# Performance work log

Hardware: AMD Instinct MI355X
Metric: run time of the kernel (lower is better)

The kernel has to match this reference:

```python
import jax, jax.numpy as jnp
import numpy as np

B, C, OUT, HD = 2, 256, 256, 32
H = C // HD                      # num_heads = 8
SCALE = HD ** -0.5
N = 40962                        # icosahedron level-6 vertices
N_TOP, TOP = 2562, 16
N_DOWN, DOWN = 2562, 19
M = N_TOP * TOP + N_DOWN * DOWN  # flattened window positions (pad row = index M)
MLP_HID = int(OUT * 2.0)
BN_EPS = 1e-5


def _build_geometry(seed=0):
    rng = np.random.default_rng(seed)
    # every vertex appears at least once; extras create overlapping patches
    flat = np.concatenate([rng.permutation(N), rng.integers(0, N, M - N)]).astype(np.int64)
    top = flat[:N_TOP * TOP].reshape(N_TOP, TOP)
    down = flat[N_TOP * TOP:].reshape(N_DOWN, DOWN)
    counts = np.bincount(flat, minlength=N)
    K = int(counts.max())
    order = np.argsort(flat, kind='stable')
    v_sorted = flat[order]
    cum = np.concatenate([[0], np.cumsum(counts)])
    pos = np.arange(M) - cum[v_sorted]          # within-group rank
    reverse = np.full((N, K), M, dtype=np.int64)  # pad -> zero row
    reverse[v_sorted, pos] = order
    cnt_inv = (1.0 / counts).astype(np.float32)
    return top, down, reverse, cnt_inv


def setup_inputs() -> dict:
    key = jax.random.key(0)
    ks = jax.random.split(key, 8)
    top, down, reverse, cnt_inv = _build_geometry(0)
    s_in, s_out, s_hid = C ** -0.5, OUT ** -0.5, MLP_HID ** -0.5
    return {
        'x': jax.random.normal(ks[0], (B, C, N), jnp.float32),
        'Wqkv': jax.random.normal(ks[1], (C, 3 * C), jnp.float32) * s_in,
        'bqkv': jnp.zeros((3 * C,), jnp.float32),
        'Wproj': jax.random.normal(ks[2], (C, OUT), jnp.float32) * s_in,
        'bproj': jnp.zeros((OUT,), jnp.float32),
        'Wres': jax.random.normal(ks[3], (C, OUT), jnp.float32) * s_in,
        'bres': jnp.zeros((OUT,), jnp.float32),
        'Wm1': jax.random.normal(ks[4], (OUT, MLP_HID), jnp.float32) * s_out,
        'bm1': jnp.zeros((MLP_HID,), jnp.float32),
        'Wm2': jax.random.normal(ks[5], (MLP_HID, OUT), jnp.float32) * s_hid,
        'bm2': jnp.zeros((OUT,), jnp.float32),
        'gamma': jnp.ones((OUT,), jnp.float32),
        'beta': jnp.zeros((OUT,), jnp.float32),
        'cnt_inv': jnp.asarray(cnt_inv),
        'top_idx': jnp.asarray(top),
        'down_idx': jnp.asarray(down),
        'reverse_idx': jnp.asarray(reverse),
    }


def reference(x, Wqkv, bqkv, Wproj, bproj, Wres, bres, Wm1, bm1, Wm2, bm2,
              gamma, beta, cnt_inv, top_idx, down_idx, reverse_idx):
    xt = jnp.transpose(x, (0, 2, 1))                      # B,N,C
    res = xt @ Wres + bres                                # B,N,OUT
    qkv = (xt @ Wqkv + bqkv).reshape(B, N, 3, H, HD)
    qkv = jnp.transpose(qkv, (2, 0, 3, 1, 4))             # 3,B,H,N,hd
    q, k, v = qkv[0] * SCALE, qkv[1], qkv[2]

    def win_attn(idx):
        qw, kw, vw = q[:, :, idx], k[:, :, idx], v[:, :, idx]   # B,H,nw,w,hd
        a = jax.nn.softmax(jnp.einsum('bhnjc,bhnkc->bhnjk', qw, kw), axis=-1)
        return jnp.einsum('bhnjk,bhnkc->bhnjc', a, vw)

    x_top = win_attn(top_idx).reshape(B, H, N_TOP * TOP, HD)
    x_down = win_attn(down_idx).reshape(B, H, N_DOWN * DOWN, HD)
    xw = jnp.concatenate([x_top, x_down], axis=2)         # B,H,M,hd
    xw = jnp.concatenate([xw, jnp.zeros((B, H, 1, HD), xw.dtype)], axis=2)  # pad row
    xg = xw[:, :, reverse_idx, :]                         # B,H,N,K,hd
    xa = (xg * cnt_inv[None, None, :, None, None]).sum(axis=3)  # B,H,N,hd
    xf = jnp.transpose(xa, (0, 2, 1, 3)).reshape(B, N, C)

    out = xf @ Wproj + bproj + res                        # B,N,OUT
    res2 = (out @ Wm1 + bm1) @ Wm2 + bm2                  # no activation (faithful)

    out_t = jnp.transpose(out, (0, 2, 1))                 # B,OUT,N
    r2t = jnp.transpose(res2, (0, 2, 1))
    mean = r2t.mean(axis=(0, 2), keepdims=True)
    var = r2t.var(axis=(0, 2), keepdims=True)             # biased, batch stats
    bn = (r2t - mean) * jax.lax.rsqrt(var + BN_EPS)
    bn = bn * gamma[None, :, None] + beta[None, :, None]
    return out_t + bn
```

## Files before the change

### kernel.cpp

```cpp
#include <hip/hip_runtime.h>
#include <stdint.h>

typedef unsigned short u16;
typedef __bf16 bf16x8 __attribute__((ext_vector_type(8)));
typedef float f32x4 __attribute__((ext_vector_type(4)));

#define B_    2
#define C_    256
#define N_    40962
#define BN_   (B_ * N_)
#define H_    8
#define HD_   32
#define NTOP  2562
#define TOPW  16
#define NDOWN 2562
#define DOWNW 19
#define M_    (NTOP*TOPW + NDOWN*DOWNW)
#define SCALE_ 0.17677669529663687f
#define BN_EPS 1e-5f

__device__ __forceinline__ float b2f(u16 u) {
    union { uint32_t i; float f; } v; v.i = ((uint32_t)u) << 16; return v.f;
}
__device__ __forceinline__ u16 f2b(float f) {
    union { float f; uint32_t i; } v; v.f = f;
    uint32_t r = v.i + 0x7fffu + ((v.i >> 16) & 1u);
    return (u16)(r >> 16);
}
__device__ __forceinline__ float ld(const void* p, size_t i, int isf32) {
    return isf32 ? ((const float*)p)[i] : b2f(((const u16*)p)[i]);
}

__device__ __forceinline__ int xcd_swz_1281(int bx) {
    const int q = 160, r = 1;
    int xcd = bx & 7, o = bx >> 3;
    return (xcd < r ? xcd * (q + 1) : r * (q + 1) + (xcd - r) * q) + o;
}

__global__ void probe_k(const void* __restrict__ x, int* __restrict__ flag) {
    int lane = threadIdx.x;
    u16 v = ((const u16*)x)[2 * lane];
    int e = (v >> 7) & 0xff;
    bool ok = (e >= 118 && e <= 134);
    unsigned long long m = __ballot(ok);
    if (lane == 0) *flag = (__popcll(m) < 32) ? 1 : 0;
}

__global__ void wcat_k(const void* __restrict__ Wqkv, const void* __restrict__ Wres,
                       const void* __restrict__ Wproj,
                       u16* __restrict__ WcatT, u16* __restrict__ WprojT,
                       const int* __restrict__ flag) {
    const int f = *flag;
    int k = blockIdx.x, t = threadIdx.x;
    for (int j = t; j < 768; j += 256) WcatT[(size_t)j * 256 + k] = f2b(ld(Wqkv, (size_t)k * 768 + j, f));
    WcatT[(size_t)(768 + t) * 256 + k] = f2b(ld(Wres, (size_t)k * 256 + t, f));
    WprojT[(size_t)t * 256 + k] = f2b(ld(Wproj, (size_t)k * 256 + t, f));
}

__global__ void biasprep_k(const void* bqkv, const void* bres, const void* bproj,
                           float* bias_cat, float* bias_proj, const int* __restrict__ flag) {
    const int f = *flag;
    int g = blockIdx.x * 256 + threadIdx.x;
    if (g < 768) bias_cat[g] = ld(bqkv, g, f);
    else if (g < 1024) bias_cat[g] = ld(bres, g - 768, f);
    else if (g < 1280) bias_proj[g - 1024] = ld(bproj, g - 1024, f);
}

__global__ __launch_bounds__(256) void wf_k(const void* __restrict__ Wm1, const void* __restrict__ Wm2,
                                            u16* __restrict__ WfT, const int* __restrict__ flag) {
    const int f = *flag;
    __shared__ float row[512];
    int i = blockIdx.x, t = threadIdx.x;
    row[t] = ld(Wm1, (size_t)i * 512 + t, f);
    row[t + 256] = ld(Wm1, (size_t)i * 512 + 256 + t, f);
    __syncthreads();
    float acc = 0.f;
    for (int k = 0; k < 512; ++k) acc += row[k] * ld(Wm2, (size_t)k * 256 + t, f);
    WfT[(size_t)t * 256 + i] = f2b(acc);
}

__global__ void bf_k(const void* bm1, const void* __restrict__ Wm2, const void* bm2,
                     float* bf, const int* __restrict__ flag) {
    const int f = *flag;
    int t = threadIdx.x;
    float acc = ld(bm2, t, f);
    for (int k = 0; k < 512; ++k) acc += ld(bm1, k, f) * ld(Wm2, (size_t)k * 256 + t, f);
    bf[t] = acc;
}

__global__ __launch_bounds__(256) void gemm_qkv_k(
    const void* __restrict__ x, const u16* __restrict__ WcatT,
    const float* __restrict__ bias, u16* __restrict__ Out, const int* __restrict__ flag)
{
    const int isf32 = *flag;
    __shared__ __align__(16) u16 As[64][264];
    const int tid = threadIdx.x;
    const int bx = xcd_swz_1281(blockIdx.x);
    const int R0 = bx * 64;
    const int wave = tid >> 6, lane = tid & 63;
    const int quad = lane >> 4, mrow = lane & 15;

    const bool fastA = (R0 + 64 <= N_) || (R0 >= N_ && R0 + 64 <= BN_);
    if (fastA) {
        const int b = (R0 >= N_) ? 1 : 0;
        const int nn = R0 - b * N_;
        const int k = tid;
        if (isf32) {
            const float* xp = (const float*)x + (size_t)(b * 256 + k) * N_ + nn;
#pragma unroll
            for (int j = 0; j < 32; ++j) {
                float2 v = *reinterpret_cast<const float2*>(xp + 2 * j);
                As[2 * j][k] = f2b(v.x);
                As[2 * j + 1][k] = f2b(v.y);
            }
        } else {
            const u16* xp = (const u16*)x + (size_t)(b * 256 + k) * N_ + nn;
#pragma unroll
            for (int j = 0; j < 32; ++j) {
                uint32_t v = *reinterpret_cast<const uint32_t*>(xp + 2 * j);
                As[2 * j][k] = (u16)v;
                As[2 * j + 1][k] = (u16)(v >> 16);
            }
        }
    } else {
        const int n = tid & 63;
        const int kg = tid >> 6;
        const int g = R0 + n;
        const bool valid = (g < BN_);
        const int b = (g >= N_) ? 1 : 0;
        const int nn = g - b * N_;
#pragma unroll
        for (int j = 0; j < 8; ++j) {
            const int k0 = kg * 8 + j * 32;
            u16 tmp[8];
            if (valid) {
#pragma unroll
                for (int i = 0; i < 8; ++i) tmp[i] = f2b(ld(x, (size_t)(b * 256 + k0 + i) * N_ + nn, isf32));
            } else {
#pragma unroll
                for (int i = 0; i < 8; ++i) tmp[i] = 0;
            }
            *reinterpret_cast<uint4*>(&As[n][k0]) = *reinterpret_cast<const uint4*>(tmp);
        }
    }
    __syncthreads();

    for (int ct = 0; ct < 16; ++ct) {
        const int col = ct * 64 + wave * 16 + mrow;
        const u16* bp = WcatT + (size_t)col * 256 + quad * 8;
        uint4 breg[8];
#pragma unroll
        for (int kc = 0; kc < 8; ++kc) breg[kc] = *reinterpret_cast<const uint4*>(bp + kc * 32);
        f32x4 acc[4] = {f32x4{0,0,0,0}, f32x4{0,0,0,0}, f32x4{0,0,0,0}, f32x4{0,0,0,0}};
#pragma unroll
        for (int kc = 0; kc < 8; ++kc) {
            bf16x8 bfrag = *reinterpret_cast<const bf16x8*>(&breg[kc]);
#pragma unroll
            for (int t2 = 0; t2 < 4; ++t2) {
                bf16x8 afrag = *reinterpret_cast<const bf16x8*>(&As[t2 * 16 + mrow][kc * 32 + quad * 8]);
                acc[t2] = __builtin_amdgcn_mfma_f32_16x16x32_bf16(afrag, bfrag, acc[t2], 0, 0, 0);
            }
        }
        const float bcol = bias[col];
#pragma unroll
        for (int t2 = 0; t2 < 4; ++t2) {
#pragma unroll
            for (int r = 0; r < 4; ++r) {
                int row = R0 + t2 * 16 + quad * 4 + r;
                if (row < BN_) {
                    Out[(size_t)row * 1024 + col] = f2b(acc[t2][r] + bcol);
                }
            }
        }
    }
}

template<bool ADD_RES, bool OUT_F32>
__global__ __launch_bounds__(256) void gemm_k(
    const u16* __restrict__ A, int ldA, const u16* __restrict__ Bt,
    const float* __restrict__ bias,
    const u16* __restrict__ resp, int ldRes,
    void* __restrict__ Out, int ldOut, int Rtot)
{
    __shared__ __align__(16) u16 As[64][264];
    const int tid = threadIdx.x;
    const int bx = xcd_swz_1281(blockIdx.x);
    const int R0 = bx * 64;
    const int wave = tid >> 6, lane = tid & 63;
    const int quad = lane >> 4, mrow = lane & 15;

#pragma unroll
    for (int it = 0; it < 8; ++it) {
        int e = it * 256 + tid;
        int row = e >> 5, ks = (e & 31) * 8;
        uint4 v = make_uint4(0u, 0u, 0u, 0u);
        if (R0 + row < Rtot)
            v = *reinterpret_cast<const uint4*>(A + (size_t)(R0 + row) * ldA + ks);
        *reinterpret_cast<uint4*>(&As[row][ks]) = v;
    }
    __syncthreads();

    for (int ct = 0; ct < 4; ++ct) {
        const int col = ct * 64 + wave * 16 + mrow;
        const u16* bp = Bt + (size_t)col * 256 + quad * 8;
        uint4 breg[8];
#pragma unroll
        for (int kc = 0; kc < 8; ++kc) breg[kc] = *reinterpret_cast<const uint4*>(bp + kc * 32);
        f32x4 acc[4] = {f32x4{0,0,0,0}, f32x4{0,0,0,0}, f32x4{0,0,0,0}, f32x4{0,0,0,0}};
#pragma unroll
        for (int kc = 0; kc < 8; ++kc) {
            bf16x8 bfrag = *reinterpret_cast<const bf16x8*>(&breg[kc]);
#pragma unroll
            for (int t2 = 0; t2 < 4; ++t2) {
                bf16x8 afrag = *reinterpret_cast<const bf16x8*>(&As[t2 * 16 + mrow][kc * 32 + quad * 8]);
                acc[t2] = __builtin_amdgcn_mfma_f32_16x16x32_bf16(afrag, bfrag, acc[t2], 0, 0, 0);
            }
        }
        const float bcol = bias[col];
#pragma unroll
        for (int t2 = 0; t2 < 4; ++t2) {
#pragma unroll
            for (int r = 0; r < 4; ++r) {
                int row = R0 + t2 * 16 + quad * 4 + r;
                if (row < Rtot) {
                    float v = acc[t2][r] + bcol;
                    if (ADD_RES) v += b2f(resp[(size_t)row * ldRes + col]);
                    if (OUT_F32) ((float*)Out)[(size_t)row * ldOut + col] = v;
                    else         ((u16*)Out)[(size_t)row * ldOut + col] = f2b(v);
                }
            }
        }
    }
}

template<int W>
__global__ __launch_bounds__(256) void attn_k(const u16* __restrict__ qkv, const int* __restrict__ widx,
                                              u16* __restrict__ xw, int mbase)
{
    const int w = blockIdx.x, b = blockIdx.y;
    const int tid = threadIdx.x;
    __shared__ int wi[W];
    __shared__ __align__(16) float Ks[W][H_][36];
    __shared__ __align__(16) float Vs[W][H_][36];
    if (tid < W) wi[tid] = widx[w * W + tid];
    __syncthreads();
    for (int e = tid; e < W * 32; e += 256) {
        int j = e >> 5, seg = e & 31;
        size_t base = ((size_t)(b * N_ + wi[j])) * 1024 + 256 + seg * 8;
        uint4 kv = *reinterpret_cast<const uint4*>(qkv + base);
        uint4 vv = *reinterpret_cast<const uint4*>(qkv + base + 256);
        int h = seg >> 2, c0 = (seg & 3) * 8;
        const u16* kp = (const u16*)&kv; const u16* vp = (const u16*)&vv;
#pragma unroll
        for (int t = 0; t < 8; ++t) {
            Ks[j][h][c0 + t] = b2f(kp[t]);
            Vs[j][h][c0 + t] = b2f(vp[t]);
        }
    }
    __syncthreads();

    if (tid < W * H_) {
        const int j = tid >> 3, h = tid & 7;
        float qr[32];
        {
            size_t qb = ((size_t)(b * N_ + wi[j])) * 1024 + h * 32;
#pragma unroll
            for (int s4 = 0; s4 < 4; ++s4) {
                uint4 qv = *reinterpret_cast<const uint4*>(qkv + qb + s4 * 8);
                const u16* qp = (const u16*)&qv;
#pragma unroll
                for (int t = 0; t < 8; ++t) qr[s4 * 8 + t] = b2f(qp[t]) * SCALE_;
            }
        }
        float p[W];
        float mx = -1e30f;
#pragma unroll
        for (int jj = 0; jj < W; ++jj) {
            const float* kr = &Ks[jj][h][0];
            float s = 0.f;
#pragma unroll
            for (int c = 0; c < 32; ++c) s += qr[c] * kr[c];
            p[jj] = s;
            mx = fmaxf(mx, s);
        }
        float sum = 0.f;
#pragma unroll
        for (int jj = 0; jj < W; ++jj) { p[jj] = __expf(p[jj] - mx); sum += p[jj]; }
        const float inv = 1.0f / sum;
        float o[32];
#pragma unroll
        for (int c = 0; c < 32; ++c) o[c] = 0.f;
#pragma unroll
        for (int jj = 0; jj < W; ++jj) {
            const float pj = p[jj];
            const float* vr = &Vs[jj][h][0];
#pragma unroll
            for (int c = 0; c < 32; ++c) o[c] += pj * vr[c];
        }
        const int m = mbase + w * W + j;
        size_t off = ((size_t)b * (M_ + 1) + m) * 256 + h * 32;
#pragma unroll
        for (int s4 = 0; s4 < 4; ++s4) {
            uint32_t w0 = (uint32_t)f2b(o[s4 * 8 + 0] * inv) | ((uint32_t)f2b(o[s4 * 8 + 1] * inv) << 16);
            uint32_t w1 = (uint32_t)f2b(o[s4 * 8 + 2] * inv) | ((uint32_t)f2b(o[s4 * 8 + 3] * inv) << 16);
            uint32_t w2 = (uint32_t)f2b(o[s4 * 8 + 4] * inv) | ((uint32_t)f2b(o[s4 * 8 + 5] * inv) << 16);
            uint32_t w3 = (uint32_t)f2b(o[s4 * 8 + 6] * inv) | ((uint32_t)f2b(o[s4 * 8 + 7] * inv) << 16);
            *reinterpret_cast<uint4*>(xw + off + s4 * 8) = make_uint4(w0, w1, w2, w3);
        }
    }
}

__global__ __launch_bounds__(256) void gather_k(const u16* __restrict__ xw, const int* __restrict__ rev,
                                                const void* __restrict__ cnt_inv, u16* __restrict__ xfp,
                                                int K, const int* __restrict__ flag)
{
    const int f = *flag;
    int gid = blockIdx.x * 4 + (threadIdx.x >> 6);
    if (gid >= BN_) return;
    int b = (gid >= N_) ? 1 : 0;
    int n = gid - b * N_;
    int c4 = (threadIdx.x & 63) * 4;
    float a0 = 0, a1 = 0, a2 = 0, a3 = 0;
    const int* rp = rev + (size_t)n * K;
    for (int k = 0; k < K; ++k) {
        int idx = rp[k];
        if (idx < M_) {
            ushort4 v = *reinterpret_cast<const ushort4*>(xw + ((size_t)b * (M_ + 1) + idx) * 256 + c4);
            a0 += b2f(v.x); a1 += b2f(v.y); a2 += b2f(v.z); a3 += b2f(v.w);
        }
    }
    float ci = ld(cnt_inv, n, f);
    ushort4 o;
    o.x = f2b(a0 * ci); o.y = f2b(a1 * ci); o.z = f2b(a2 * ci); o.w = f2b(a3 * ci);
    *reinterpret_cast<ushort4*>(xfp + (size_t)gid * 1024 + c4) = o;
}

#define STATS_BLOCKS 512
__global__ __launch_bounds__(256) void stats_k(const float* __restrict__ res2, float* __restrict__ sums) {
    const int tid = threadIdx.x;
    const int c4 = (tid & 63) * 4;
    const int rsub = tid >> 6;
    float s[4] = {0.f, 0.f, 0.f, 0.f};
    float q[4] = {0.f, 0.f, 0.f, 0.f};
    for (int r = blockIdx.x * 4 + rsub; r < BN_; r += STATS_BLOCKS * 4) {
        float4 v = *reinterpret_cast<const float4*>(res2 + (size_t)r * 256 + c4);
        s[0] += v.x; q[0] += v.x * v.x;
        s[1] += v.y; q[1] += v.y * v.y;
        s[2] += v.z; q[2] += v.z * v.z;
        s[3] += v.w; q[3] += v.w * v.w;
    }
    __shared__ float rs[256][4];
    __shared__ float rq[256][4];
#pragma unroll
    for (int j = 0; j < 4; ++j) { rs[tid][j] = s[j]; rq[tid][j] = q[j]; }
    __syncthreads();
    if (tid < 64) {
#pragma unroll
        for (int j = 0; j < 4; ++j) {
            float a = rs[tid][j] + rs[tid + 64][j] + rs[tid + 128][j] + rs[tid + 192][j];
            float b = rq[tid][j] + rq[tid + 64][j] + rq[tid + 128][j] + rq[tid + 192][j];
            atomicAdd(&sums[c4 + j], a);
            atomicAdd(&sums[256 + c4 + j], b);
        }
    }
}

__global__ void bnfin_k(const float* sums, const void* gamma, const void* beta, float* ss,
                        const int* __restrict__ flag) {
    const int f = *flag;
    int c = threadIdx.x;
    float mean = sums[c] * (1.0f / BN_);
    float var = sums[256 + c] * (1.0f / BN_) - mean * mean;
    float inv = rsqrtf(fmaxf(var, 0.f) + BN_EPS);
    float sc = ld(gamma, c, f) * inv;
    ss[c] = sc;
    ss[256 + c] = ld(beta, c, f) - mean * sc;
}

__global__ __launch_bounds__(256) void final_k(const u16* __restrict__ outb, const float* __restrict__ res2,
                                               const float* __restrict__ ss, void* __restrict__ y,
                                               const int* __restrict__ flag)
{
    const int isf32 = *flag;
    __shared__ __align__(16) float tile[64][65];
    const int n0 = blockIdx.x * 64, o0 = blockIdx.y * 64, b = blockIdx.z;
    const int tid = threadIdx.x;
    {
        const int ln = tid >> 2, os = (tid & 3) * 16;
        int n = n0 + ln;
        if (n < N_) {
            size_t base = ((size_t)(b * N_ + n)) * 256 + o0 + os;
            uint4 ov0 = *reinterpret_cast<const uint4*>(outb + base);
            uint4 ov1 = *reinterpret_cast<const uint4*>(outb + base + 8);
            const u16* op = (const u16*)&ov0;
            const u16* op1 = (const u16*)&ov1;
            float4 rv[4];
#pragma unroll
            for (int q = 0; q < 4; ++q) rv[q] = *reinterpret_cast<const float4*>(res2 + base + q * 4);
            const float* rp = (const float*)&rv[0];
#pragma unroll
            for (int j = 0; j < 16; ++j) {
                int oc = o0 + os + j;
                float ob = (j < 8) ? b2f(op[j]) : b2f(op1[j - 8]);
                tile[ln][os + j] = ob + rp[j] * ss[oc] + ss[256 + oc];
            }
        }
    }
    __syncthreads();
    {
        const int wave = tid >> 6, lane = tid & 63;
        int n = n0 + lane;
        if (n < N_) {
            if (isf32) {
                float* yp = (float*)y;
#pragma unroll
                for (int r0 = 0; r0 < 64; r0 += 4) {
                    int r = r0 + wave;
                    int oc = o0 + r;
                    yp[((size_t)(b * 256 + oc)) * N_ + n] = tile[lane][r];
                }
            } else {
                u16* yp = (u16*)y;
#pragma unroll
                for (int r0 = 0; r0 < 64; r0 += 4) {
                    int r = r0 + wave;
                    int oc = o0 + r;
                    yp[((size_t)(b * 256 + oc)) * N_ + n] = f2b(tile[lane][r]);
                }
            }
        }
    }
}

static const size_t OFF_QKV   = 0;
static const size_t OFF_XW    = 167780352;
static const size_t OFF_SMALL = 259603456;

extern "C" void kernel_launch(void* const* d_in, const int* in_sizes, int n_in,
                              void* d_out, int out_size, void* d_ws, size_t ws_size,
                              hipStream_t stream) {
    const void* x     = d_in[0];
    const void* Wqkv  = d_in[1];
    const void* bqkv  = d_in[2];
    const void* Wproj = d_in[3];
    const void* bproj = d_in[4];
    const void* Wres  = d_in[5];
    const void* bres  = d_in[6];
    const void* Wm1   = d_in[7];
    const void* bm1   = d_in[8];
    const void* Wm2   = d_in[9];
    const void* bm2   = d_in[10];
    const void* gamma = d_in[11];
    const void* beta  = d_in[12];
    const void* cnt_inv = d_in[13];
    const int* top_idx = (const int*)d_in[14];
    const int* down_idx = (const int*)d_in[15];
    const int* rev   = (const int*)d_in[16];
    const int K = in_sizes[16] / N_;

    char* ws = (char*)d_ws;
    u16*  qkvres  = (u16*)(ws + OFF_QKV);
    float* res2   = (float*)(ws + OFF_QKV);
    u16*  xw      = (u16*)(ws + OFF_XW);
    u16*  outb    = (u16*)(ws + OFF_XW);
    u16*  WcatT   = (u16*)(ws + OFF_SMALL);
    u16*  WfT     = (u16*)(ws + OFF_SMALL + 524288);
    float* bias_cat  = (float*)(ws + OFF_SMALL + 655360);
    float* bias_proj = (float*)(ws + OFF_SMALL + 659456);
    float* bfv       = (float*)(ws + OFF_SMALL + 663552);
    float* stats     = (float*)(ws + OFF_SMALL + 667648);
    float* ssbuf     = (float*)(ws + OFF_SMALL + 671744);
    int*   flag      = (int*)(ws + OFF_SMALL + 675840);
    u16*  WprojT     = (u16*)(ws + OFF_SMALL + 679936);

    probe_k<<<1, 64, 0, stream>>>(x, flag);

    wcat_k<<<256, 256, 0, stream>>>(Wqkv, Wres, Wproj, WcatT, WprojT, flag);
    biasprep_k<<<5, 256, 0, stream>>>(bqkv, bres, bproj, bias_cat, bias_proj, flag);
    wf_k<<<256, 256, 0, stream>>>(Wm1, Wm2, WfT, flag);
    bf_k<<<1, 256, 0, stream>>>(bm1, Wm2, bm2, bfv, flag);

    gemm_qkv_k<<<1281, 256, 0, stream>>>(x, WcatT, bias_cat, qkvres, flag);

    attn_k<TOPW><<<dim3(NTOP, B_), 256, 0, stream>>>(qkvres, top_idx, xw, 0);
    attn_k<DOWNW><<<dim3(NDOWN, B_), 256, 0, stream>>>(qkvres, down_idx, xw, NTOP * TOPW);

    gather_k<<<(BN_ + 3) / 4, 256, 0, stream>>>(xw, rev, cnt_inv, qkvres, K, flag);

    gemm_k<true, false><<<1281, 256, 0, stream>>>(
        qkvres, 1024, WprojT, bias_proj, qkvres + 768, 1024, (void*)outb, 256, BN_);

    gemm_k<false, true><<<1281, 256, 0, stream>>>(
        outb, 256, WfT, bfv, nullptr, 0, (void*)res2, 256, BN_);

    (void)hipMemsetAsync(stats, 0, 512 * sizeof(float), stream);
    stats_k<<<STATS_BLOCKS, 256, 0, stream>>>(res2, stats);
    bnfin_k<<<1, 256, 0, stream>>>(stats, gamma, beta, ssbuf, flag);

    final_k<<<dim3(641, 4, 2), 256, 0, stream>>>(outb, res2, ssbuf, d_out, flag);
}
```

Before: 868.2 us.

## Fuse projection and folded MLP GEMMs into one kernel with paired column tiles

Merges the projection GEMM (plus residual) and the folded MLP GEMM into a single kernel. Each block computes its 64 rows of outb, then reloads them into shared memory and immediately computes res2. This removes one launch and keeps the reload of outb cache-hot. The QKV and fused GEMMs now load B fragments for two column tiles at once to raise memory-level parallelism, at the cost of more registers. res2 is stored with a padded 512-float row stride and offset, which doubles its footprint and may change how its accesses map to channels or banks.

Measured after the change: 981.9 us. 1.13x slower.

```diff
diff --git a/kernel.cpp b/kernel.cpp
--- a/kernel.cpp
+++ b/kernel.cpp
@@ -19,6 +19,8 @@
 #define SCALE_ 0.17677669529663687f
 #define BN_EPS 1e-5f
 
+#define RES2_IDX(row, col) ((size_t)(row) * 512 + 128 + (col))
+
 __device__ __forceinline__ float b2f(u16 u) {
     union { uint32_t i; float f; } v; v.i = ((uint32_t)u) << 16; return v.f;
 }
@@ -145,42 +147,64 @@
     }
     __syncthreads();
 
-    for (int ct = 0; ct < 16; ++ct) {
-        const int col = ct * 64 + wave * 16 + mrow;
-        const u16* bp = WcatT + (size_t)col * 256 + quad * 8;
-        uint4 breg[8];
-#pragma unroll
-        for (int kc = 0; kc < 8; ++kc) breg[kc] = *reinterpret_cast<const uint4*>(bp + kc * 32);
+    for (int cp = 0; cp < 8; ++cp) {
+        const int colA = (cp * 2) * 64 + wave * 16 + mrow;
+        const int colB = colA + 64;
+        const u16* bpA = WcatT + (size_t)colA * 256 + quad * 8;
+        const u16* bpB = WcatT + (size_t)colB * 256 + quad * 8;
+        uint4 bregA[8], bregB[8];
+#pragma unroll
+        for (int kc = 0; kc < 8; ++kc) bregA[kc] = *reinterpret_cast<const uint4*>(bpA + kc * 32);
+#pragma unroll
+        for (int kc = 0; kc < 8; ++kc) bregB[kc] = *reinterpret_cast<const uint4*>(bpB + kc * 32);
         f32x4 acc[4] = {f32x4{0,0,0,0}, f32x4{0,0,0,0}, f32x4{0,0,0,0}, f32x4{0,0,0,0}};
 #pragma unroll
         for (int kc = 0; kc < 8; ++kc) {
-            bf16x8 bfrag = *reinterpret_cast<const bf16x8*>(&breg[kc]);
+            bf16x8 bfrag = *reinterpret_cast<const bf16x8*>(&bregA[kc]);
 #pragma unroll
             for (int t2 = 0; t2 < 4; ++t2) {
                 bf16x8 afrag = *reinterpret_cast<const bf16x8*>(&As[t2 * 16 + mrow][kc * 32 + quad * 8]);
                 acc[t2] = __builtin_amdgcn_mfma_f32_16x16x32_bf16(afrag, bfrag, acc[t2], 0, 0, 0);
             }
         }
-        const float bcol = bias[col];
-#pragma unroll
-        for (int t2 = 0; t2 < 4; ++t2) {
-#pragma unroll
-            for (int r = 0; r < 4; ++r) {
-                int row = R0 + t2 * 16 + quad * 4 + r;
-                if (row < BN_) {
-                    Out[(size_t)row * 1024 + col] = f2b(acc[t2][r] + bcol);
-                }
-            }
-        }
-    }
-}
-
-template<bool ADD_RES, bool OUT_F32>
-__global__ __launch_bounds__(256) void gemm_k(
-    const u16* __restrict__ A, int ldA, const u16* __restrict__ Bt,
-    const float* __restrict__ bias,
-    const u16* __restrict__ resp, int ldRes,
-    void* __restrict__ Out, int ldOut, int Rtot)
+        {
+            const float bcol = bias[colA];
+#pragma unroll
+            for (int t2 = 0; t2 < 4; ++t2)
+#pragma unroll
+                for (int r = 0; r < 4; ++r) {
+                    int row = R0 + t2 * 16 + quad * 4 + r;
+                    if (row < BN_) Out[(size_t)row * 1024 + colA] = f2b(acc[t2][r] + bcol);
+                }
+        }
+#pragma unroll
+        for (int t2 = 0; t2 < 4; ++t2) acc[t2] = f32x4{0,0,0,0};
+#pragma unroll
+        for (int kc = 0; kc < 8; ++kc) {
+            bf16x8 bfrag = *reinterpret_cast<const bf16x8*>(&bregB[kc]);
+#pragma unroll
+            for (int t2 = 0; t2 < 4; ++t2) {
+                bf16x8 afrag = *reinterpret_cast<const bf16x8*>(&As[t2 * 16 + mrow][kc * 32 + quad * 8]);
+                acc[t2] = __builtin_amdgcn_mfma_f32_16x16x32_bf16(afrag, bfrag, acc[t2], 0, 0, 0);
+            }
+        }
+        {
+            const float bcol = bias[colB];
+#pragma unroll
+            for (int t2 = 0; t2 < 4; ++t2)
+#pragma unroll
+                for (int r = 0; r < 4; ++r) {
+                    int row = R0 + t2 * 16 + quad * 4 + r;
+                    if (row < BN_) Out[(size_t)row * 1024 + colB] = f2b(acc[t2][r] + bcol);
+                }
+        }
+    }
+}
+
+__global__ __launch_bounds__(256) void gemm_mlp_k(
+    const u16* __restrict__ xf, const u16* __restrict__ WprojT, const float* __restrict__ bproj,
+    const u16* __restrict__ resp, const u16* __restrict__ WfT, const float* __restrict__ bfv,
+    u16* __restrict__ outb, float* __restrict__ res2)
 {
     __shared__ __align__(16) u16 As[64][264];
     const int tid = threadIdx.x;
@@ -194,41 +218,133 @@
         int e = it * 256 + tid;
         int row = e >> 5, ks = (e & 31) * 8;
         uint4 v = make_uint4(0u, 0u, 0u, 0u);
-        if (R0 + row < Rtot)
-            v = *reinterpret_cast<const uint4*>(A + (size_t)(R0 + row) * ldA + ks);
+        if (R0 + row < BN_)
+            v = *reinterpret_cast<const uint4*>(xf + (size_t)(R0 + row) * 1024 + ks);
         *reinterpret_cast<uint4*>(&As[row][ks]) = v;
     }
     __syncthreads();
 
-    for (int ct = 0; ct < 4; ++ct) {
-        const int col = ct * 64 + wave * 16 + mrow;
-        const u16* bp = Bt + (size_t)col * 256 + quad * 8;
-        uint4 breg[8];
-#pragma unroll
-        for (int kc = 0; kc < 8; ++kc) breg[kc] = *reinterpret_cast<const uint4*>(bp + kc * 32);
+    for (int cp = 0; cp < 2; ++cp) {
+        const int colA = cp * 128 + wave * 16 + mrow;
+        const int colB = colA + 64;
+        const u16* bpA = WprojT + (size_t)colA * 256 + quad * 8;
+        const u16* bpB = WprojT + (size_t)colB * 256 + quad * 8;
+        uint4 bregA[8], bregB[8];
+#pragma unroll
+        for (int kc = 0; kc < 8; ++kc) bregA[kc] = *reinterpret_cast<const uint4*>(bpA + kc * 32);
+#pragma unroll
+        for (int kc = 0; kc < 8; ++kc) bregB[kc] = *reinterpret_cast<const uint4*>(bpB + kc * 32);
         f32x4 acc[4] = {f32x4{0,0,0,0}, f32x4{0,0,0,0}, f32x4{0,0,0,0}, f32x4{0,0,0,0}};
 #pragma unroll
         for (int kc = 0; kc < 8; ++kc) {
-            bf16x8 bfrag = *reinterpret_cast<const bf16x8*>(&breg[kc]);
+            bf16x8 bfrag = *reinterpret_cast<const bf16x8*>(&bregA[kc]);
 #pragma unroll
             for (int t2 = 0; t2 < 4; ++t2) {
                 bf16x8 afrag = *reinterpret_cast<const bf16x8*>(&As[t2 * 16 + mrow][kc * 32 + quad * 8]);
                 acc[t2] = __builtin_amdgcn_mfma_f32_16x16x32_bf16(afrag, bfrag, acc[t2], 0, 0, 0);
             }
         }
-        const float bcol = bias[col];
-#pragma unroll
-        for (int t2 = 0; t2 < 4; ++t2) {
-#pragma unroll
-            for (int r = 0; r < 4; ++r) {
-                int row = R0 + t2 * 16 + quad * 4 + r;
-                if (row < Rtot) {
-                    float v = acc[t2][r] + bcol;
-                    if (ADD_RES) v += b2f(resp[(size_t)row * ldRes + col]);
-                    if (OUT_F32) ((float*)Out)[(size_t)row * ldOut + col] = v;
-                    else         ((u16*)Out)[(size_t)row * ldOut + col] = f2b(v);
-                }
-            }
+        {
+            const float bcol = bproj[colA];
+#pragma unroll
+            for (int t2 = 0; t2 < 4; ++t2)
+#pragma unroll
+                for (int r = 0; r < 4; ++r) {
+                    int row = R0 + t2 * 16 + quad * 4 + r;
+                    if (row < BN_) {
+                        float v = acc[t2][r] + bcol + b2f(resp[(size_t)row * 1024 + colA]);
+                        outb[(size_t)row * 256 + colA] = f2b(v);
+                    }
+                }
+        }
+#pragma unroll
+        for (int t2 = 0; t2 < 4; ++t2) acc[t2] = f32x4{0,0,0,0};
+#pragma unroll
+        for (int kc = 0; kc < 8; ++kc) {
+            bf16x8 bfrag = *reinterpret_cast<const bf16x8*>(&bregB[kc]);
+#pragma unroll
+            for (int t2 = 0; t2 < 4; ++t2) {
+                bf16x8 afrag = *reinterpret_cast<const bf16x8*>(&As[t2 * 16 + mrow][kc * 32 + quad * 8]);
+                acc[t2] = __builtin_amdgcn_mfma_f32_16x16x32_bf16(afrag, bfrag, acc[t2], 0, 0, 0);
+            }
+        }
+        {
+            const float bcol = bproj[colB];
+#pragma unroll
+            for (int t2 = 0; t2 < 4; ++t2)
+#pragma unroll
+                for (int r = 0; r < 4; ++r) {
+                    int row = R0 + t2 * 16 + quad * 4 + r;
+                    if (row < BN_) {
+                        float v = acc[t2][r] + bcol + b2f(resp[(size_t)row * 1024 + colB]);
+                        outb[(size_t)row * 256 + colB] = f2b(v);
+                    }
+                }
+        }
+    }
+    __syncthreads();
+
+#pragma unroll
+    for (int it = 0; it < 8; ++it) {
+        int e = it * 256 + tid;
+        int row = e >> 5, ks = (e & 31) * 8;
+        uint4 v = make_uint4(0u, 0u, 0u, 0u);
+        if (R0 + row < BN_)
+            v = *reinterpret_cast<const uint4*>(outb + (size_t)(R0 + row) * 256 + ks);
+        *reinterpret_cast<uint4*>(&As[row][ks]) = v;
+    }
+    __syncthreads();
+
+    for (int cp = 0; cp < 2; ++cp) {
+        const int colA = cp * 128 + wave * 16 + mrow;
+        const int colB = colA + 64;
+        const u16* bpA = WfT + (size_t)colA * 256 + quad * 8;
+        const u16* bpB = WfT + (size_t)colB * 256 + quad * 8;
+        uint4 bregA[8], bregB[8];
+#pragma unroll
+        for (int kc = 0; kc < 8; ++kc) bregA[kc] = *reinterpret_cast<const uint4*>(bpA + kc * 32);
+#pragma unroll
+        for (int kc = 0; kc < 8; ++kc) bregB[kc] = *reinterpret_cast<const uint4*>(bpB + kc * 32);
+        f32x4 acc[4] = {f32x4{0,0,0,0}, f32x4{0,0,0,0}, f32x4{0,0,0,0}, f32x4{0,0,0,0}};
+#pragma unroll
+        for (int kc = 0; kc < 8; ++kc) {
+            bf16x8 bfrag = *reinterpret_cast<const bf16x8*>(&bregA[kc]);
+#pragma unroll
+            for (int t2 = 0; t2 < 4; ++t2) {
+                bf16x8 afrag = *reinterpret_cast<const bf16x8*>(&As[t2 * 16 + mrow][kc * 32 + quad * 8]);
+                acc[t2] = __builtin_amdgcn_mfma_f32_16x16x32_bf16(afrag, bfrag, acc[t2], 0, 0, 0);
+            }
+        }
+        {
+            const float bcol = bfv[colA];
+#pragma unroll
+            for (int t2 = 0; t2 < 4; ++t2)
+#pragma unroll
+                for (int r = 0; r < 4; ++r) {
+                    int row = R0 + t2 * 16 + quad * 4 + r;
+                    if (row < BN_) res2[RES2_IDX(row, colA)] = acc[t2][r] + bcol;
+                }
+        }
+#pragma unroll
+        for (int t2 = 0; t2 < 4; ++t2) acc[t2] = f32x4{0,0,0,0};
+#pragma unroll
+        for (int kc = 0; kc < 8; ++kc) {
+            bf16x8 bfrag = *reinterpret_cast<const bf16x8*>(&bregB[kc]);
+#pragma unroll
+            for (int t2 = 0; t2 < 4; ++t2) {
+                bf16x8 afrag = *reinterpret_cast<const bf16x8*>(&As[t2 * 16 + mrow][kc * 32 + quad * 8]);
+                acc[t2] = __builtin_amdgcn_mfma_f32_16x16x32_bf16(afrag, bfrag, acc[t2], 0, 0, 0);
+            }
+        }
+        {
+            const float bcol = bfv[colB];
+#pragma unroll
+            for (int t2 = 0; t2 < 4; ++t2)
+#pragma unroll
+                for (int r = 0; r < 4; ++r) {
+                    int row = R0 + t2 * 16 + quad * 4 + r;
+                    if (row < BN_) res2[RES2_IDX(row, colB)] = acc[t2][r] + bcol;
+                }
         }
     }
 }
@@ -343,7 +459,7 @@
     float s[4] = {0.f, 0.f, 0.f, 0.f};
     float q[4] = {0.f, 0.f, 0.f, 0.f};
     for (int r = blockIdx.x * 4 + rsub; r < BN_; r += STATS_BLOCKS * 4) {
-        float4 v = *reinterpret_cast<const float4*>(res2 + (size_t)r * 256 + c4);
+        float4 v = *reinterpret_cast<const float4*>(res2 + RES2_IDX(r, c4));
         s[0] += v.x; q[0] += v.x * v.x;
         s[1] += v.y; q[1] += v.y * v.y;
         s[2] += v.z; q[2] += v.z * v.z;
@@ -389,14 +505,16 @@
         const int ln = tid >> 2, os = (tid & 3) * 16;
         int n = n0 + ln;
         if (n < N_) {
-            size_t base = ((size_t)(b * N_ + n)) * 256 + o0 + os;
+            size_t row = (size_t)(b * N_ + n);
+            size_t base = row * 256 + o0 + os;
             uint4 ov0 = *reinterpret_cast<const uint4*>(outb + base);
             uint4 ov1 = *reinterpret_cast<const uint4*>(outb + base + 8);
             const u16* op = (const u16*)&ov0;
             const u16* op1 = (const u16*)&ov1;
             float4 rv[4];
 #pragma unroll
-            for (int q = 0; q < 4; ++q) rv[q] = *reinterpret_cast<const float4*>(res2 + base + q * 4);
+            for (int q = 0; q < 4; ++q)
+                rv[q] = *reinterpret_cast<const float4*>(res2 + RES2_IDX(row, o0 + os + q * 4));
             const float* rp = (const float*)&rv[0];
 #pragma unroll
             for (int j = 0; j < 16; ++j) {
@@ -487,11 +605,8 @@
 
     gather_k<<<(BN_ + 3) / 4, 256, 0, stream>>>(xw, rev, cnt_inv, qkvres, K, flag);
 
-    gemm_k<true, false><<<1281, 256, 0, stream>>>(
-        qkvres, 1024, WprojT, bias_proj, qkvres + 768, 1024, (void*)outb, 256, BN_);
-
-    gemm_k<false, true><<<1281, 256, 0, stream>>>(
-        outb, 256, WfT, bfv, nullptr, 0, (void*)res2, 256, BN_);
+    gemm_mlp_k<<<1281, 256, 0, stream>>>(
+        qkvres, WprojT, bias_proj, qkvres + 768, WfT, bfv, outb, res2);
 
     (void)hipMemsetAsync(stats, 0, 512 * sizeof(float), stream);
     stats_k<<<STATS_BLOCKS, 256, 0, stream>>>(res2, stats);
```
